# Kernel tuning notes

Measured on AMD Instinct MI355X. Metric: run time of the kernel, lower is better.

## Reference

```python
import jax, jax.numpy as jnp
import numpy as np

B, C, H, W = 8, 384, 32, 32
HEADS, DIM_HEAD = 6, 64
INNER = HEADS * DIM_HEAD  # 384


def setup_inputs() -> dict:
    key = jax.random.key(0)
    ks = jax.random.split(key, 6)
    s = 0.02
    return {
        "query": jax.random.normal(ks[0], (B, C, H, W), jnp.float32),
        "context": jax.random.normal(ks[1], (B, C, H, W), jnp.float32),
        "Wq": jax.random.normal(ks[2], (INNER, C), jnp.float32) * s,
        "Wk": jax.random.normal(ks[3], (INNER, C), jnp.float32) * s,
        "Wv": jax.random.normal(ks[4], (INNER, C), jnp.float32) * s,
        "Wo": jax.random.normal(ks[5], (C, INNER), jnp.float32) * s,
        "bo": jnp.zeros((C,), jnp.float32),
    }


def reference(query, context, Wq, Wk, Wv, Wo, bo):
    scale = DIM_HEAD ** (-0.5)
    b, _, h, w = query.shape
    n = h * w  # tokens
    # 1x1 convs == channel-wise linear projections
    q = jnp.einsum('bchw,oc->bohw', query, Wq)
    k = jnp.einsum('bchw,oc->bohw', context, Wk)
    v = jnp.einsum('bchw,oc->bohw', context, Wv)
    # split heads: [B, heads, dim_head, N]
    q = q.reshape(b, HEADS, DIM_HEAD, n)
    k = k.reshape(b, HEADS, DIM_HEAD, n)
    v = v.reshape(b, HEADS, DIM_HEAD, n)
    # attn[b,h,i,j] = sum_d q[b,h,d,i] k[b,h,d,j] * scale
    attn = jax.nn.softmax(jnp.einsum('bhdn,bhdm->bhnm', q, k) * scale, axis=-1)
    # out[b,h,i,d] = sum_j attn[b,h,i,j] v[b,h,d,j]
    out = jnp.einsum('bhnm,bhdm->bhdn', attn, v)  # [B, heads, dim_head, N]
    out = out.reshape(b, INNER, h, w)
    out = jnp.einsum('bchw,oc->bohw', out, Wo) + bo[None, :, None, None]
    attn_map = attn.mean(axis=(1, 2)).reshape(b, h, w)
    return out, attn_map
```

## Files before the change

kernel.cpp:

```cpp
#include <hip/hip_runtime.h>

#define BATCH 8
#define CCH   384
#define NTOK  1024
#define HEADS 6
#define DHEAD 64
#define SCALE 0.125f

typedef __bf16 bf16x8 __attribute__((ext_vector_type(8)));
typedef float  f32x4  __attribute__((ext_vector_type(4)));

#define MFMA16(a, b, c) __builtin_amdgcn_mfma_f32_16x16x32_bf16((a), (b), (c), 0, 0, 0)

__device__ __forceinline__ short f2b(float x) {
    unsigned u = __float_as_uint(x);
    u += 0x7fffu + ((u >> 16) & 1u);
    return (short)(u >> 16);
}

__device__ __forceinline__ void gld_lds16(const short* gp, short* lp) {
    __builtin_amdgcn_global_load_lds(
        (const __attribute__((address_space(1))) void*)gp,
        (__attribute__((address_space(3))) void*)lp, 16, 0, 0);
}

__device__ __forceinline__ void stage_tile(const short* gbase, size_t gstride,
                                           short* lbase, int wv, int lane) {
#pragma unroll
    for (int t = 0; t < 2; ++t) {
        const int row = t * 8 + (lane >> 3);
        const int c   = (lane & 7) ^ (row & 7);
        gld_lds16(gbase + (size_t)(wv * 16 + row) * gstride + c * 8,
                  lbase + (wv * 16 + t * 8) * 64);
    }
}

__device__ __forceinline__ bf16x8 frag_read(const short* lbase, int row, int c) {
    const int pc = c ^ (row & 7);
    return *(const bf16x8*)(lbase + row * 64 + pc * 8);
}

__global__ __launch_bounds__(256) void xpose_both(
    const float* __restrict__ Xq, const float* __restrict__ Xc,
    short* __restrict__ Xtq, short* __restrict__ Xtc)
{
    __shared__ float tile[64][65];
    const int tid = threadIdx.x;
    const int zz = blockIdx.z;
    const float* X = (zz < 8) ? Xq : Xc;
    short* Xt      = (zz < 8) ? Xtq : Xtc;
    const int b = zz & 7, n0 = blockIdx.x * 64, c0 = blockIdx.y * 64;
    const int tx = tid & 15, ty = tid >> 4;
#pragma unroll
    for (int rr = 0; rr < 4; ++rr) {
        const int c = rr * 16 + ty;
        float4 v = *(const float4*)&X[((size_t)(b * CCH + c0 + c)) * NTOK + n0 + tx * 4];
        tile[c][tx * 4 + 0] = v.x; tile[c][tx * 4 + 1] = v.y;
        tile[c][tx * 4 + 2] = v.z; tile[c][tx * 4 + 3] = v.w;
    }
    __syncthreads();
    const int n = tid >> 2, cb = (tid & 3) * 16;
    short tmp[16];
#pragma unroll
    for (int cc = 0; cc < 16; ++cc) tmp[cc] = f2b(tile[cb + cc][n]);
    short* dst = &Xt[((size_t)(b * NTOK + n0 + n)) * CCH + c0 + cb];
    *(int4*)dst = *(int4*)&tmp[0];
    *(int4*)(dst + 8) = *(int4*)&tmp[8];
}

__global__ __launch_bounds__(256) void convert_w(
    const float* __restrict__ w0, const float* __restrict__ w1,
    const float* __restrict__ w2, const float* __restrict__ w3,
    short* __restrict__ o0, short* __restrict__ o1,
    short* __restrict__ o2, short* __restrict__ o3)
{
    const int idx = blockIdx.x * 256 + threadIdx.x;
    const int which = blockIdx.y;
    const float* s = which == 0 ? w0 : which == 1 ? w1 : which == 2 ? w2 : w3;
    short* d       = which == 0 ? o0 : which == 1 ? o1 : which == 2 ? o2 : o3;
    float4 v = ((const float4*)s)[idx];
    short4 o = make_short4(f2b(v.x), f2b(v.y), f2b(v.z), f2b(v.w));
    ((short4*)d)[idx] = o;
}

__global__ __launch_bounds__(256) void proj_qkv(
    const short* __restrict__ xtq, const short* __restrict__ xtc,
    const short* __restrict__ wq, const short* __restrict__ wk,
    const short* __restrict__ wv,
    short* __restrict__ qout, short* __restrict__ kout, short* __restrict__ vout)
{
    __shared__ __align__(16) short Bst[6][64 * 64];
    const int tid = threadIdx.x, lane = tid & 63;
    const int l15 = tid & 15, quad = (tid >> 4) & 3, wv4 = tid >> 6;
    const int id = blockIdx.x;
    const int b = id & 7, q = id >> 3;
    const int which = q % 3, rr = q / 3;
    const int c0 = (rr % 6) * 64, t0 = (rr / 6) * 64;

    const short* xa   = (which == 0) ? xtq : xtc;
    const short* Wsel = (which == 0) ? wq : (which == 1) ? wk : wv;

    const short* Abase, *Bbase;
    if (which < 2) {
        Abase = xa + ((size_t)(b * NTOK + t0)) * CCH;
        Bbase = Wsel + (size_t)c0 * CCH;
    } else {
        Abase = Wsel + (size_t)c0 * CCH;
        Bbase = xa + ((size_t)(b * NTOK + t0)) * CCH;
    }

    const short* arow = Abase + (size_t)(wv4 * 16 + l15) * CCH + quad * 8;
    bf16x8 Af[12];
#pragma unroll
    for (int kc = 0; kc < 12; ++kc) Af[kc] = *(const bf16x8*)(arow + kc * 32);
#pragma unroll
    for (int kt = 0; kt < 6; ++kt)
        stage_tile(Bbase + kt * 64, CCH, &Bst[kt][0], wv4, lane);
    __syncthreads();

    f32x4 acc[4] = {{0,0,0,0},{0,0,0,0},{0,0,0,0},{0,0,0,0}};
#pragma unroll
    for (int kc = 0; kc < 12; ++kc) {
        bf16x8 a = Af[kc];
#pragma unroll
        for (int ns = 0; ns < 4; ++ns) {
            bf16x8 bb = frag_read(&Bst[kc >> 1][0], ns * 16 + l15,
                                  ((kc & 1) << 2) | quad);
            acc[ns] = MFMA16(a, bb, acc[ns]);
        }
    }

    if (which < 2) {
        short* out = (which == 0) ? qout : kout;
#pragma unroll
        for (int ns = 0; ns < 4; ++ns)
#pragma unroll
            for (int r = 0; r < 4; ++r) {
                const int tok = t0 + wv4 * 16 + quad * 4 + r;
                out[((size_t)(b * NTOK + tok)) * CCH + c0 + ns * 16 + l15] =
                    f2b(acc[ns][r]);
            }
    } else {
#pragma unroll
        for (int ns = 0; ns < 4; ++ns)
#pragma unroll
            for (int r = 0; r < 4; ++r) {
                const int ch = c0 + wv4 * 16 + quad * 4 + r;
                vout[((size_t)(b * CCH + ch)) * NTOK + t0 + ns * 16 + l15] =
                    f2b(acc[ns][r]);
            }
    }
}

__global__ __launch_bounds__(256) void o_proj(
    const short* __restrict__ wo, const short* __restrict__ omid,
    const float* __restrict__ bias, float* __restrict__ Y)
{
    __shared__ __align__(16) short Bst[6][64 * 64];
    const int tid = threadIdx.x, lane = tid & 63;
    const int l15 = tid & 15, quad = (tid >> 4) & 3, wv4 = tid >> 6;
    const int id = blockIdx.x;
    const int b = id & 7, rr = id >> 3;
    const int m0 = (rr % 6) * 64, n0 = (rr / 6) * 64;

    const short* Abase = wo + (size_t)m0 * CCH;
    const short* Bbase = omid + ((size_t)(b * NTOK + n0)) * CCH;

    const short* arow = Abase + (size_t)(wv4 * 16 + l15) * CCH + quad * 8;
    bf16x8 Af[12];
#pragma unroll
    for (int kc = 0; kc < 12; ++kc) Af[kc] = *(const bf16x8*)(arow + kc * 32);
#pragma unroll
    for (int kt = 0; kt < 6; ++kt)
        stage_tile(Bbase + kt * 64, CCH, &Bst[kt][0], wv4, lane);
    __syncthreads();

    f32x4 acc[4] = {{0,0,0,0},{0,0,0,0},{0,0,0,0},{0,0,0,0}};
#pragma unroll
    for (int kc = 0; kc < 12; ++kc) {
        bf16x8 a = Af[kc];
#pragma unroll
        for (int ns = 0; ns < 4; ++ns) {
            bf16x8 bb = frag_read(&Bst[kc >> 1][0], ns * 16 + l15,
                                  ((kc & 1) << 2) | quad);
            acc[ns] = MFMA16(a, bb, acc[ns]);
        }
    }
#pragma unroll
    for (int ns = 0; ns < 4; ++ns)
#pragma unroll
        for (int r = 0; r < 4; ++r) {
            const int ch = m0 + wv4 * 16 + quad * 4 + r;
            Y[((size_t)(b * CCH + ch)) * NTOK + n0 + ns * 16 + l15] =
                acc[ns][r] + bias[ch];
        }
}

__global__ __launch_bounds__(256) void attn(
    const short* __restrict__ qt, const short* __restrict__ kt,
    const short* __restrict__ vc, short* __restrict__ omid,
    float* __restrict__ amap)
{
    __shared__ __align__(16) short Kst[2][64 * 64];
    __shared__ __align__(16) short Vst[2][64 * 64];
    __shared__ __align__(16) short Pst[4][16][64];
    __shared__ float colbuf[2][4][64];

    const int tid = threadIdx.x, lane = tid & 63;
    const int l15 = tid & 15, quad = (tid >> 4) & 3, wv = tid >> 6;
    const int id = blockIdx.x;
    const int b = id & 7, rr = id >> 3;
    const int h = rr % 6, i0 = (rr / 6) * 64;

    const size_t hoff = (size_t)b * NTOK * CCH + h * DHEAD;
    const short* Kg = kt + hoff;
    const short* Vg = vc + ((size_t)(b * CCH + h * DHEAD)) * NTOK;

    const short* qp = qt + hoff + (size_t)(i0 + wv * 16 + l15) * CCH + quad * 8;
    const bf16x8 qa0 = *(const bf16x8*)qp;
    const bf16x8 qa1 = *(const bf16x8*)(qp + 32);

    stage_tile(Kg, CCH, Kst[0], wv, lane);
    __syncthreads();

    float den[4] = {0.f, 0.f, 0.f, 0.f};
    for (int jt = 0; jt < 16; ++jt) {
        const int cur = jt & 1;
        if (jt < 15)
            stage_tile(Kg + (size_t)(jt + 1) * 64 * CCH, CCH, Kst[cur ^ 1], wv, lane);
        f32x4 s[4] = {{0,0,0,0},{0,0,0,0},{0,0,0,0},{0,0,0,0}};
#pragma unroll
        for (int ns = 0; ns < 4; ++ns) {
            const int row = ns * 16 + l15;
            bf16x8 k0 = frag_read(Kst[cur], row, quad);
            bf16x8 k1 = frag_read(Kst[cur], row, quad + 4);
            s[ns] = MFMA16(qa0, k0, s[ns]);
            s[ns] = MFMA16(qa1, k1, s[ns]);
        }
#pragma unroll
        for (int ns = 0; ns < 4; ++ns)
#pragma unroll
            for (int r = 0; r < 4; ++r)
                den[r] += __expf(s[ns][r] * SCALE);
        __syncthreads();
    }
#pragma unroll
    for (int r = 0; r < 4; ++r) {
        den[r] += __shfl_xor(den[r], 1);
        den[r] += __shfl_xor(den[r], 2);
        den[r] += __shfl_xor(den[r], 4);
        den[r] += __shfl_xor(den[r], 8);
    }
    float rden[4];
#pragma unroll
    for (int r = 0; r < 4; ++r) rden[r] = 1.0f / den[r];

    stage_tile(Kg, CCH, Kst[0], wv, lane);
    stage_tile(Vg, NTOK, Vst[0], wv, lane);
    __syncthreads();

    f32x4 oacc[4] = {{0,0,0,0},{0,0,0,0},{0,0,0,0},{0,0,0,0}};
    for (int jt = 0; jt < 16; ++jt) {
        const int cur = jt & 1;
        if (jt < 15) {
            stage_tile(Kg + (size_t)(jt + 1) * 64 * CCH, CCH, Kst[cur ^ 1], wv, lane);
            stage_tile(Vg + (size_t)(jt + 1) * 64, NTOK, Vst[cur ^ 1], wv, lane);
        }
        f32x4 s[4] = {{0,0,0,0},{0,0,0,0},{0,0,0,0},{0,0,0,0}};
#pragma unroll
        for (int ns = 0; ns < 4; ++ns) {
            const int row = ns * 16 + l15;
            bf16x8 k0 = frag_read(Kst[cur], row, quad);
            bf16x8 k1 = frag_read(Kst[cur], row, quad + 4);
            s[ns] = MFMA16(qa0, k0, s[ns]);
            s[ns] = MFMA16(qa1, k1, s[ns]);
        }
        float p[4][4];
#pragma unroll
        for (int ns = 0; ns < 4; ++ns)
#pragma unroll
            for (int r = 0; r < 4; ++r)
                p[ns][r] = __expf(s[ns][r] * SCALE) * rden[r];

#pragma unroll
        for (int ns = 0; ns < 4; ++ns) {
            float cs = p[ns][0] + p[ns][1] + p[ns][2] + p[ns][3];
            cs += __shfl_xor(cs, 16);
            cs += __shfl_xor(cs, 32);
            if (quad == 0) colbuf[cur][wv][ns * 16 + l15] = cs;
        }

#pragma unroll
        for (int ns = 0; ns < 4; ++ns) {
            const int c = ns * 2 + (l15 >> 3);
#pragma unroll
            for (int r = 0; r < 4; ++r) {
                const int row = quad * 4 + r;
                Pst[wv][row][((c ^ (row & 7)) << 3) | (l15 & 7)] = f2b(p[ns][r]);
            }
        }
        asm volatile("" ::: "memory");
        const int pc0 = quad ^ (l15 & 7);
        const int pc1 = (quad + 4) ^ (l15 & 7);
        bf16x8 pa0 = *(const bf16x8*)&Pst[wv][l15][pc0 * 8];
        bf16x8 pa1 = *(const bf16x8*)&Pst[wv][l15][pc1 * 8];
        asm volatile("" ::: "memory");

#pragma unroll
        for (int ds = 0; ds < 4; ++ds) {
            const int row = ds * 16 + l15;
            bf16x8 v0 = frag_read(Vst[cur], row, quad);
            bf16x8 v1 = frag_read(Vst[cur], row, quad + 4);
            oacc[ds] = MFMA16(pa0, v0, oacc[ds]);
            oacc[ds] = MFMA16(pa1, v1, oacc[ds]);
        }
        __syncthreads();
        if (tid < 64) {
            const float t = colbuf[cur][0][tid] + colbuf[cur][1][tid]
                          + colbuf[cur][2][tid] + colbuf[cur][3][tid];
            atomicAdd(amap + (size_t)b * NTOK + jt * 64 + tid,
                      t * (1.0f / (HEADS * NTOK)));
        }
    }

#pragma unroll
    for (int ds = 0; ds < 4; ++ds)
#pragma unroll
        for (int r = 0; r < 4; ++r) {
            const int i = i0 + wv * 16 + quad * 4 + r;
            omid[((size_t)(b * NTOK + i)) * CCH + h * DHEAD + ds * 16 + l15] =
                f2b(oacc[ds][r]);
        }
}

extern "C" void kernel_launch(void* const* d_in, const int* in_sizes, int n_in,
                              void* d_out, int out_size, void* d_ws, size_t ws_size,
                              hipStream_t stream)
{
    const float* query   = (const float*)d_in[0];
    const float* context = (const float*)d_in[1];
    const float* Wq      = (const float*)d_in[2];
    const float* Wk      = (const float*)d_in[3];
    const float* Wv      = (const float*)d_in[4];
    const float* Wo      = (const float*)d_in[5];
    const float* bo      = (const float*)d_in[6];

    float* out = (float*)d_out;
    const size_t out_elems = (size_t)BATCH * CCH * NTOK;
    float* attn_map = out + out_elems;

    short* ws = (short*)d_ws;
    const size_t XT = (size_t)BATCH * NTOK * CCH;
    const size_t WSZ = (size_t)CCH * CCH;
    short* xtq  = ws;
    short* xtc  = xtq + XT;
    short* wqb  = xtc + XT;
    short* wkb  = wqb + WSZ;
    short* wvb  = wkb + WSZ;
    short* wob  = wvb + WSZ;
    short* qtb  = wob + WSZ;
    short* ktb  = qtb + XT;
    short* vcb  = ktb + XT;
    short* omid = vcb + XT;

    const dim3 blk(256);

    xpose_both<<<dim3(16, 6, 16), blk, 0, stream>>>(query, context, xtq, xtc);
    convert_w<<<dim3(144, 4), blk, 0, stream>>>(Wq, Wk, Wv, Wo, wqb, wkb, wvb, wob);

    proj_qkv<<<dim3(2304), blk, 0, stream>>>(xtq, xtc, wqb, wkb, wvb,
                                             qtb, ktb, vcb);

    hipMemsetAsync(attn_map, 0, (size_t)BATCH * NTOK * sizeof(float), stream);

    attn<<<dim3(768), blk, 0, stream>>>(qtb, ktb, vcb, omid, attn_map);

    o_proj<<<dim3(768), blk, 0, stream>>>(wob, omid, bo, out);
}
```

Baseline: 167.9 us.

## Merge prep kernels, retile projections to 128x128, cache exp scores in attention

```diff
diff --git a/kernel.cpp b/kernel.cpp
--- a/kernel.cpp
+++ b/kernel.cpp
@@ -34,183 +34,213 @@
                   lbase + (wv * 16 + t * 8) * 64);
     }
 }
-
 __device__ __forceinline__ bf16x8 frag_read(const short* lbase, int row, int c) {
     const int pc = c ^ (row & 7);
     return *(const bf16x8*)(lbase + row * 64 + pc * 8);
 }
 
-__global__ __launch_bounds__(256) void xpose_both(
+__device__ __forceinline__ void stage_panel32(const short* g, short* l,
+                                              int wv, int lane) {
+#pragma unroll
+    for (int t = 0; t < 2; ++t) {
+        const int rg  = wv * 2 + t;
+        const int row = rg * 16 + (lane >> 2);
+        gld_lds16(g + (size_t)row * CCH + (lane & 3) * 8, l + rg * 512);
+    }
+}
+
+__device__ __forceinline__ void gemm128_core(
+    const short* __restrict__ Ag, const short* __restrict__ Bg,
+    short* Ast, short* Bst, f32x4 acc[4][4])
+{
+    const int tid = threadIdx.x, lane = tid & 63;
+    const int l15 = tid & 15, quad = (tid >> 4) & 3, wv = tid >> 6;
+    const int wi = (wv >> 1) * 64, wj = (wv & 1) * 64;
+
+    stage_panel32(Ag, Ast, wv, lane);
+    stage_panel32(Bg, Bst, wv, lane);
+    __syncthreads();
+
+#pragma unroll 2
+    for (int kc = 0; kc < 12; ++kc) {
+        const int cur = kc & 1;
+        if (kc < 11) {
+            stage_panel32(Ag + (kc + 1) * 32, Ast + (cur ^ 1) * 4096, wv, lane);
+            stage_panel32(Bg + (kc + 1) * 32, Bst + (cur ^ 1) * 4096, wv, lane);
+        }
+        bf16x8 a[4], b[4];
+#pragma unroll
+        for (int s = 0; s < 4; ++s) {
+            a[s] = *(const bf16x8*)(Ast + cur * 4096 + (wi + s * 16 + l15) * 32 + quad * 8);
+            b[s] = *(const bf16x8*)(Bst + cur * 4096 + (wj + s * 16 + l15) * 32 + quad * 8);
+        }
+#pragma unroll
+        for (int si = 0; si < 4; ++si)
+#pragma unroll
+            for (int sj = 0; sj < 4; ++sj)
+                acc[si][sj] = MFMA16(a[si], b[sj], acc[si][sj]);
+        __syncthreads();
+    }
+}
+
+__global__ __launch_bounds__(256) void prep(
     const float* __restrict__ Xq, const float* __restrict__ Xc,
-    short* __restrict__ Xtq, short* __restrict__ Xtc)
-{
-    __shared__ float tile[64][65];
-    const int tid = threadIdx.x;
-    const int zz = blockIdx.z;
-    const float* X = (zz < 8) ? Xq : Xc;
-    short* Xt      = (zz < 8) ? Xtq : Xtc;
-    const int b = zz & 7, n0 = blockIdx.x * 64, c0 = blockIdx.y * 64;
-    const int tx = tid & 15, ty = tid >> 4;
-#pragma unroll
-    for (int rr = 0; rr < 4; ++rr) {
-        const int c = rr * 16 + ty;
-        float4 v = *(const float4*)&X[((size_t)(b * CCH + c0 + c)) * NTOK + n0 + tx * 4];
-        tile[c][tx * 4 + 0] = v.x; tile[c][tx * 4 + 1] = v.y;
-        tile[c][tx * 4 + 2] = v.z; tile[c][tx * 4 + 3] = v.w;
-    }
-    __syncthreads();
-    const int n = tid >> 2, cb = (tid & 3) * 16;
-    short tmp[16];
-#pragma unroll
-    for (int cc = 0; cc < 16; ++cc) tmp[cc] = f2b(tile[cb + cc][n]);
-    short* dst = &Xt[((size_t)(b * NTOK + n0 + n)) * CCH + c0 + cb];
-    *(int4*)dst = *(int4*)&tmp[0];
-    *(int4*)(dst + 8) = *(int4*)&tmp[8];
-}
-
-__global__ __launch_bounds__(256) void convert_w(
     const float* __restrict__ w0, const float* __restrict__ w1,
     const float* __restrict__ w2, const float* __restrict__ w3,
+    short* __restrict__ Xtq, short* __restrict__ Xtc,
     short* __restrict__ o0, short* __restrict__ o1,
-    short* __restrict__ o2, short* __restrict__ o3)
-{
-    const int idx = blockIdx.x * 256 + threadIdx.x;
-    const int which = blockIdx.y;
-    const float* s = which == 0 ? w0 : which == 1 ? w1 : which == 2 ? w2 : w3;
-    short* d       = which == 0 ? o0 : which == 1 ? o1 : which == 2 ? o2 : o3;
-    float4 v = ((const float4*)s)[idx];
-    short4 o = make_short4(f2b(v.x), f2b(v.y), f2b(v.z), f2b(v.w));
-    ((short4*)d)[idx] = o;
-}
-
-__global__ __launch_bounds__(256) void proj_qkv(
+    short* __restrict__ o2, short* __restrict__ o3,
+    float* __restrict__ amap)
+{
+    __shared__ float tile[64][65];
+    const int id = blockIdx.x, tid = threadIdx.x;
+    if (id < 1536) {
+        const int zz = id % 16, t = id / 16;
+        const int n0 = (t % 16) * 64, c0 = (t / 16) * 64;
+        const float* X = (zz < 8) ? Xq : Xc;
+        short* Xt      = (zz < 8) ? Xtq : Xtc;
+        const int b = zz & 7;
+        const int tx = tid & 15, ty = tid >> 4;
+#pragma unroll
+        for (int rr = 0; rr < 4; ++rr) {
+            const int c = rr * 16 + ty;
+            float4 v = *(const float4*)&X[((size_t)(b * CCH + c0 + c)) * NTOK + n0 + tx * 4];
+            tile[c][tx * 4 + 0] = v.x; tile[c][tx * 4 + 1] = v.y;
+            tile[c][tx * 4 + 2] = v.z; tile[c][tx * 4 + 3] = v.w;
+        }
+        __syncthreads();
+        const int n = tid >> 2, cb = (tid & 3) * 16;
+        short tmp[16];
+#pragma unroll
+        for (int cc = 0; cc < 16; ++cc) tmp[cc] = f2b(tile[cb + cc][n]);
+        short* dst = &Xt[((size_t)(b * NTOK + n0 + n)) * CCH + c0 + cb];
+        *(int4*)dst = *(int4*)&tmp[0];
+        *(int4*)(dst + 8) = *(int4*)&tmp[8];
+    } else if (id < 2112) {
+        const int w = id - 1536;
+        const int which = w / 144;
+        const int idx = (w % 144) * 256 + tid;
+        const float* s = which == 0 ? w0 : which == 1 ? w1 : which == 2 ? w2 : w3;
+        short* d       = which == 0 ? o0 : which == 1 ? o1 : which == 2 ? o2 : o3;
+        float4 v = ((const float4*)s)[idx];
+        short4 o = make_short4(f2b(v.x), f2b(v.y), f2b(v.z), f2b(v.w));
+        ((short4*)d)[idx] = o;
+    } else {
+        const int o = (id - 2112) * 1024 + tid * 4;
+        float4 z = {0.f, 0.f, 0.f, 0.f};
+        *(float4*)&amap[o] = z;
+    }
+}
+
+__global__ __launch_bounds__(256, 2) void gemm_qkv(
     const short* __restrict__ xtq, const short* __restrict__ xtc,
     const short* __restrict__ wq, const short* __restrict__ wk,
-    const short* __restrict__ wv,
+    const short* __restrict__ wvm,
     short* __restrict__ qout, short* __restrict__ kout, short* __restrict__ vout)
 {
-    __shared__ __align__(16) short Bst[6][64 * 64];
-    const int tid = threadIdx.x, lane = tid & 63;
-    const int l15 = tid & 15, quad = (tid >> 4) & 3, wv4 = tid >> 6;
+    __shared__ __align__(16) short Ast[2][4096];
+    __shared__ __align__(16) short Bst[2][4096];
     const int id = blockIdx.x;
-    const int b = id & 7, q = id >> 3;
-    const int which = q % 3, rr = q / 3;
-    const int c0 = (rr % 6) * 64, t0 = (rr / 6) * 64;
-
-    const short* xa   = (which == 0) ? xtq : xtc;
-    const short* Wsel = (which == 0) ? wq : (which == 1) ? wk : wv;
-
-    const short* Abase, *Bbase;
+    const int b = id & 7, r = id >> 3;
+    const int which = r / 24, tt = r % 24;
+
+    const short *Ag, *Bg;
+    short* out;
+    size_t obase;
+    int ostride;
     if (which < 2) {
-        Abase = xa + ((size_t)(b * NTOK + t0)) * CCH;
-        Bbase = Wsel + (size_t)c0 * CCH;
+        const int it = tt / 3, jt = tt % 3;
+        const short* x = (which == 0) ? xtq : xtc;
+        const short* W = (which == 0) ? wq : wk;
+        Ag = x + ((size_t)(b * NTOK + it * 128)) * CCH;
+        Bg = W + (size_t)(jt * 128) * CCH;
+        out = (which == 0) ? qout : kout;
+        obase = ((size_t)(b * NTOK + it * 128)) * CCH + jt * 128;
+        ostride = CCH;
     } else {
-        Abase = Wsel + (size_t)c0 * CCH;
-        Bbase = xa + ((size_t)(b * NTOK + t0)) * CCH;
-    }
-
-    const short* arow = Abase + (size_t)(wv4 * 16 + l15) * CCH + quad * 8;
-    bf16x8 Af[12];
-#pragma unroll
-    for (int kc = 0; kc < 12; ++kc) Af[kc] = *(const bf16x8*)(arow + kc * 32);
-#pragma unroll
-    for (int kt = 0; kt < 6; ++kt)
-        stage_tile(Bbase + kt * 64, CCH, &Bst[kt][0], wv4, lane);
-    __syncthreads();
-
-    f32x4 acc[4] = {{0,0,0,0},{0,0,0,0},{0,0,0,0},{0,0,0,0}};
-#pragma unroll
-    for (int kc = 0; kc < 12; ++kc) {
-        bf16x8 a = Af[kc];
-#pragma unroll
-        for (int ns = 0; ns < 4; ++ns) {
-            bf16x8 bb = frag_read(&Bst[kc >> 1][0], ns * 16 + l15,
-                                  ((kc & 1) << 2) | quad);
-            acc[ns] = MFMA16(a, bb, acc[ns]);
-        }
-    }
-
-    if (which < 2) {
-        short* out = (which == 0) ? qout : kout;
-#pragma unroll
-        for (int ns = 0; ns < 4; ++ns)
-#pragma unroll
-            for (int r = 0; r < 4; ++r) {
-                const int tok = t0 + wv4 * 16 + quad * 4 + r;
-                out[((size_t)(b * NTOK + tok)) * CCH + c0 + ns * 16 + l15] =
-                    f2b(acc[ns][r]);
-            }
-    } else {
-#pragma unroll
-        for (int ns = 0; ns < 4; ++ns)
-#pragma unroll
-            for (int r = 0; r < 4; ++r) {
-                const int ch = c0 + wv4 * 16 + quad * 4 + r;
-                vout[((size_t)(b * CCH + ch)) * NTOK + t0 + ns * 16 + l15] =
-                    f2b(acc[ns][r]);
-            }
-    }
-}
-
-__global__ __launch_bounds__(256) void o_proj(
+        const int ct = tt % 3, nt = tt / 3;
+        Ag = wvm + (size_t)(ct * 128) * CCH;
+        Bg = xtc + ((size_t)(b * NTOK + nt * 128)) * CCH;
+        out = vout;
+        obase = ((size_t)(b * CCH + ct * 128)) * NTOK + nt * 128;
+        ostride = NTOK;
+    }
+
+    f32x4 z4 = {0.f, 0.f, 0.f, 0.f};
+    f32x4 acc[4][4];
+#pragma unroll
+    for (int si = 0; si < 4; ++si)
+#pragma unroll
+        for (int sj = 0; sj < 4; ++sj) acc[si][sj] = z4;
+
+    gemm128_core(Ag, Bg, &Ast[0][0], &Bst[0][0], acc);
+
+    const int tid = threadIdx.x;
+    const int l15 = tid & 15, quad = (tid >> 4) & 3, wv = tid >> 6;
+    const int wi = (wv >> 1) * 64, wj = (wv & 1) * 64;
+#pragma unroll
+    for (int si = 0; si < 4; ++si)
+#pragma unroll
+        for (int sj = 0; sj < 4; ++sj)
+#pragma unroll
+            for (int rr = 0; rr < 4; ++rr)
+                out[obase + (size_t)(wi + si * 16 + quad * 4 + rr) * ostride
+                    + wj + sj * 16 + l15] = f2b(acc[si][sj][rr]);
+}
+
+__global__ __launch_bounds__(256, 2) void o_proj(
     const short* __restrict__ wo, const short* __restrict__ omid,
     const float* __restrict__ bias, float* __restrict__ Y)
 {
-    __shared__ __align__(16) short Bst[6][64 * 64];
-    const int tid = threadIdx.x, lane = tid & 63;
-    const int l15 = tid & 15, quad = (tid >> 4) & 3, wv4 = tid >> 6;
+    __shared__ __align__(16) short Ast[2][4096];
+    __shared__ __align__(16) short Bst[2][4096];
     const int id = blockIdx.x;
-    const int b = id & 7, rr = id >> 3;
-    const int m0 = (rr % 6) * 64, n0 = (rr / 6) * 64;
-
-    const short* Abase = wo + (size_t)m0 * CCH;
-    const short* Bbase = omid + ((size_t)(b * NTOK + n0)) * CCH;
-
-    const short* arow = Abase + (size_t)(wv4 * 16 + l15) * CCH + quad * 8;
-    bf16x8 Af[12];
-#pragma unroll
-    for (int kc = 0; kc < 12; ++kc) Af[kc] = *(const bf16x8*)(arow + kc * 32);
-#pragma unroll
-    for (int kt = 0; kt < 6; ++kt)
-        stage_tile(Bbase + kt * 64, CCH, &Bst[kt][0], wv4, lane);
-    __syncthreads();
-
-    f32x4 acc[4] = {{0,0,0,0},{0,0,0,0},{0,0,0,0},{0,0,0,0}};
-#pragma unroll
-    for (int kc = 0; kc < 12; ++kc) {
-        bf16x8 a = Af[kc];
-#pragma unroll
-        for (int ns = 0; ns < 4; ++ns) {
-            bf16x8 bb = frag_read(&Bst[kc >> 1][0], ns * 16 + l15,
-                                  ((kc & 1) << 2) | quad);
-            acc[ns] = MFMA16(a, bb, acc[ns]);
-        }
-    }
-#pragma unroll
-    for (int ns = 0; ns < 4; ++ns)
-#pragma unroll
-        for (int r = 0; r < 4; ++r) {
-            const int ch = m0 + wv4 * 16 + quad * 4 + r;
-            Y[((size_t)(b * CCH + ch)) * NTOK + n0 + ns * 16 + l15] =
-                acc[ns][r] + bias[ch];
-        }
-}
-
-__global__ __launch_bounds__(256) void attn(
+    const int b = id & 7, r = id >> 3;
+    const int ct = r % 3, nt = r / 3;
+
+    const short* Ag = wo + (size_t)(ct * 128) * CCH;
+    const short* Bg = omid + ((size_t)(b * NTOK + nt * 128)) * CCH;
+
+    f32x4 z4 = {0.f, 0.f, 0.f, 0.f};
+    f32x4 acc[4][4];
+#pragma unroll
+    for (int si = 0; si < 4; ++si)
+#pragma unroll
+        for (int sj = 0; sj < 4; ++sj) acc[si][sj] = z4;
+
+    gemm128_core(Ag, Bg, &Ast[0][0], &Bst[0][0], acc);
+
+    const int tid = threadIdx.x;
+    const int l15 = tid & 15, quad = (tid >> 4) & 3, wv = tid >> 6;
+    const int wi = (wv >> 1) * 64, wj = (wv & 1) * 64;
+#pragma unroll
+    for (int si = 0; si < 4; ++si) {
+#pragma unroll
+        for (int rr = 0; rr < 4; ++rr) {
+            const int ch = ct * 128 + wi + si * 16 + quad * 4 + rr;
+            const float bv = bias[ch];
+#pragma unroll
+            for (int sj = 0; sj < 4; ++sj)
+                Y[((size_t)(b * CCH + ch)) * NTOK + nt * 128 + wj + sj * 16 + l15] =
+                    acc[si][sj][rr] + bv;
+        }
+    }
+}
+
+__global__ __launch_bounds__(256, 2) void attn(
     const short* __restrict__ qt, const short* __restrict__ kt,
     const short* __restrict__ vc, short* __restrict__ omid,
     float* __restrict__ amap)
 {
-    __shared__ __align__(16) short Kst[2][64 * 64];
-    __shared__ __align__(16) short Vst[2][64 * 64];
+    __shared__ __align__(16) short KV[2][64 * 64];
     __shared__ __align__(16) short Pst[4][16][64];
     __shared__ float colbuf[2][4][64];
 
     const int tid = threadIdx.x, lane = tid & 63;
     const int l15 = tid & 15, quad = (tid >> 4) & 3, wv = tid >> 6;
     const int id = blockIdx.x;
-    const int b = id & 7, rr = id >> 3;
-    const int h = rr % 6, i0 = (rr / 6) * 64;
+    const int b = id & 7, rr_ = id >> 3;
+    const int h = rr_ % 6, i0 = (rr_ / 6) * 64;
 
     const size_t hoff = (size_t)b * NTOK * CCH + h * DHEAD;
     const short* Kg = kt + hoff;
@@ -220,28 +250,39 @@
     const bf16x8 qa0 = *(const bf16x8*)qp;
     const bf16x8 qa1 = *(const bf16x8*)(qp + 32);
 
-    stage_tile(Kg, CCH, Kst[0], wv, lane);
+    int ebuf[16][8];
+
+    stage_tile(Kg, CCH, KV[0], wv, lane);
     __syncthreads();
 
     float den[4] = {0.f, 0.f, 0.f, 0.f};
     for (int jt = 0; jt < 16; ++jt) {
         const int cur = jt & 1;
         if (jt < 15)
-            stage_tile(Kg + (size_t)(jt + 1) * 64 * CCH, CCH, Kst[cur ^ 1], wv, lane);
-        f32x4 s[4] = {{0,0,0,0},{0,0,0,0},{0,0,0,0},{0,0,0,0}};
+            stage_tile(Kg + (size_t)(jt + 1) * 64 * CCH, CCH, KV[cur ^ 1], wv, lane);
+        f32x4 z4 = {0.f, 0.f, 0.f, 0.f};
+        f32x4 s[4] = {z4, z4, z4, z4};
 #pragma unroll
         for (int ns = 0; ns < 4; ++ns) {
             const int row = ns * 16 + l15;
-            bf16x8 k0 = frag_read(Kst[cur], row, quad);
-            bf16x8 k1 = frag_read(Kst[cur], row, quad + 4);
+            bf16x8 k0 = frag_read(KV[cur], row, quad);
+            bf16x8 k1 = frag_read(KV[cur], row, quad + 4);
             s[ns] = MFMA16(qa0, k0, s[ns]);
             s[ns] = MFMA16(qa1, k1, s[ns]);
         }
 #pragma unroll
-        for (int ns = 0; ns < 4; ++ns)
-#pragma unroll
-            for (int r = 0; r < 4; ++r)
-                den[r] += __expf(s[ns][r] * SCALE);
+        for (int ns = 0; ns < 4; ++ns) {
+#pragma unroll
+            for (int p = 0; p < 2; ++p) {
+                const float e0 = __expf(s[ns][2 * p]     * SCALE);
+                const float e1 = __expf(s[ns][2 * p + 1] * SCALE);
+                den[2 * p]     += e0;
+                den[2 * p + 1] += e1;
+                ebuf[jt][ns * 2 + p] =
+                    (int)((unsigned short)f2b(e0)) |
+                    ((int)((unsigned short)f2b(e1)) << 16);
+            }
+        }
         __syncthreads();
     }
 #pragma unroll
@@ -255,49 +296,35 @@
 #pragma unroll
     for (int r = 0; r < 4; ++r) rden[r] = 1.0f / den[r];
 
-    stage_tile(Kg, CCH, Kst[0], wv, lane);
-    stage_tile(Vg, NTOK, Vst[0], wv, lane);
+    stage_tile(Vg, NTOK, KV[0], wv, lane);
     __syncthreads();
 
-    f32x4 oacc[4] = {{0,0,0,0},{0,0,0,0},{0,0,0,0},{0,0,0,0}};
+    f32x4 z4o = {0.f, 0.f, 0.f, 0.f};
+    f32x4 oacc[4] = {z4o, z4o, z4o, z4o};
     for (int jt = 0; jt < 16; ++jt) {
         const int cur = jt & 1;
-        if (jt < 15) {
-            stage_tile(Kg + (size_t)(jt + 1) * 64 * CCH, CCH, Kst[cur ^ 1], wv, lane);
-            stage_tile(Vg + (size_t)(jt + 1) * 64, NTOK, Vst[cur ^ 1], wv, lane);
-        }
-        f32x4 s[4] = {{0,0,0,0},{0,0,0,0},{0,0,0,0},{0,0,0,0}};
+        if (jt < 15)
+            stage_tile(Vg + (size_t)(jt + 1) * 64, NTOK, KV[cur ^ 1], wv, lane);
+
 #pragma unroll
         for (int ns = 0; ns < 4; ++ns) {
-            const int row = ns * 16 + l15;
-            bf16x8 k0 = frag_read(Kst[cur], row, quad);
-            bf16x8 k1 = frag_read(Kst[cur], row, quad + 4);
-            s[ns] = MFMA16(qa0, k0, s[ns]);
-            s[ns] = MFMA16(qa1, k1, s[ns]);
-        }
-        float p[4][4];
-#pragma unroll
-        for (int ns = 0; ns < 4; ++ns)
-#pragma unroll
-            for (int r = 0; r < 4; ++r)
-                p[ns][r] = __expf(s[ns][r] * SCALE) * rden[r];
-
-#pragma unroll
-        for (int ns = 0; ns < 4; ++ns) {
-            float cs = p[ns][0] + p[ns][1] + p[ns][2] + p[ns][3];
+            const int c = ns * 2 + (l15 >> 3);
+            float cs = 0.f;
+#pragma unroll
+            for (int p = 0; p < 2; ++p) {
+                const int w = ebuf[jt][ns * 2 + p];
+                const float v0 = __uint_as_float(((unsigned)w) << 16);
+                const float v1 = __uint_as_float(((unsigned)w) & 0xffff0000u);
+                cs = fmaf(v0, rden[2 * p], cs);
+                cs = fmaf(v1, rden[2 * p + 1], cs);
+                const int r0 = quad * 4 + 2 * p;
+                const int r1 = r0 + 1;
+                Pst[wv][r0][((c ^ (r0 & 7)) << 3) | (l15 & 7)] = (short)(w & 0xffff);
+                Pst[wv][r1][((c ^ (r1 & 7)) << 3) | (l15 & 7)] = (short)(((unsigned)w) >> 16);
+            }
             cs += __shfl_xor(cs, 16);
             cs += __shfl_xor(cs, 32);
             if (quad == 0) colbuf[cur][wv][ns * 16 + l15] = cs;
-        }
-
-#pragma unroll
-        for (int ns = 0; ns < 4; ++ns) {
-            const int c = ns * 2 + (l15 >> 3);
-#pragma unroll
-            for (int r = 0; r < 4; ++r) {
-                const int row = quad * 4 + r;
-                Pst[wv][row][((c ^ (row & 7)) << 3) | (l15 & 7)] = f2b(p[ns][r]);
-            }
         }
         asm volatile("" ::: "memory");
         const int pc0 = quad ^ (l15 & 7);
@@ -309,8 +336,8 @@
 #pragma unroll
         for (int ds = 0; ds < 4; ++ds) {
             const int row = ds * 16 + l15;
-            bf16x8 v0 = frag_read(Vst[cur], row, quad);
-            bf16x8 v1 = frag_read(Vst[cur], row, quad + 4);
+            bf16x8 v0 = frag_read(KV[cur], row, quad);
+            bf16x8 v1 = frag_read(KV[cur], row, quad + 4);
             oacc[ds] = MFMA16(pa0, v0, oacc[ds]);
             oacc[ds] = MFMA16(pa1, v1, oacc[ds]);
         }
@@ -329,7 +356,7 @@
         for (int r = 0; r < 4; ++r) {
             const int i = i0 + wv * 16 + quad * 4 + r;
             omid[((size_t)(b * NTOK + i)) * CCH + h * DHEAD + ds * 16 + l15] =
-                f2b(oacc[ds][r]);
+                f2b(oacc[ds][r] * rden[r]);
         }
 }
 
@@ -365,15 +392,13 @@
 
     const dim3 blk(256);
 
-    xpose_both<<<dim3(16, 6, 16), blk, 0, stream>>>(query, context, xtq, xtc);
-    convert_w<<<dim3(144, 4), blk, 0, stream>>>(Wq, Wk, Wv, Wo, wqb, wkb, wvb, wob);
-
-    proj_qkv<<<dim3(2304), blk, 0, stream>>>(xtq, xtc, wqb, wkb, wvb,
-                                             qtb, ktb, vcb);
-
-    hipMemsetAsync(attn_map, 0, (size_t)BATCH * NTOK * sizeof(float), stream);
+    prep<<<dim3(2120), blk, 0, stream>>>(query, context, Wq, Wk, Wv, Wo,
+                                         xtq, xtc, wqb, wkb, wvb, wob, attn_map);
+
+    gemm_qkv<<<dim3(576), blk, 0, stream>>>(xtq, xtc, wqb, wkb, wvb,
+                                            qtb, ktb, vcb);
 
     attn<<<dim3(768), blk, 0, stream>>>(qtb, ktb, vcb, omid, attn_map);
 
-    o_proj<<<dim3(768), blk, 0, stream>>>(wob, omid, bo, out);
-}
+    o_proj<<<dim3(192), blk, 0, stream>>>(wob, omid, bo, out);
+}
```

After: 170.2 us. Within noise of the previous version (+1.4%).
